# Kernel tuning notes

Hardware: AMD Instinct MI355X
Metric: run time of the kernel (lower is better)

The kernel has to match this reference:

```python
import jax, jax.numpy as jnp
import numpy as np

# DBMLLoss hyperparameters (from cfg.LOSSES.DBML_LOSS.*)
POS_A, POS_B = 1.0, 0.5
NEG_A, NEG_B = 0.6, 0.5
MARGIN, WEIGHT = 0.1, 0.5
EPS = 1e-5


def setup_inputs() -> dict:
    key = jax.random.key(0)
    k1, k2 = jax.random.split(key)
    feats = jax.random.normal(k1, (4096, 512), dtype=jnp.float32)
    feats = feats / jnp.linalg.norm(feats, axis=1, keepdims=True)  # metric-learning embeddings are L2-normalized
    labels = jax.random.randint(k2, (4096,), 0, 100)
    return {"feats": feats, "labels": labels}


def _dbml_loss(feats, labels):
    # feats: [B, D], labels: [B] int
    B = feats.shape[0]
    ninf = jnp.array(-jnp.inf, feats.dtype)
    pinf = jnp.array(jnp.inf, feats.dtype)

    sim = feats @ feats.T  # [B, B]
    same = labels[:, None] == labels[None, :]  # [B, B]
    # pos_pair_: same label and sim < 1 - eps (drops self-similarity of normalized feats)
    pos_mask = same & (sim < 1.0 - EPS)
    neg_mask = ~same

    # full-row stats (torch.mean(sum(...)) over a scalar == the sum)
    mean_all = sim.mean(axis=1)                               # [B]
    sigma_all = ((sim - mean_all[:, None]) ** 2).sum(axis=1)  # [B]

    max_neg = jnp.max(jnp.where(neg_mask, sim, ninf), axis=1)  # [B]
    min_pos = jnp.min(jnp.where(pos_mask, sim, pinf), axis=1)  # [B]

    # adaptive selection (adaptive_neg=True branch)
    pos_sel = pos_mask & (sim - MARGIN < max_neg[:, None])
    neg_sel = neg_mask & (sim + MARGIN > min_pos[:, None])

    n_pos = pos_sel.sum(axis=1)
    n_neg = neg_sel.sum(axis=1)
    valid = (pos_mask.sum(axis=1) > 0) & (neg_mask.sum(axis=1) > 0) & (n_pos > 0) & (n_neg > 0)

    sel = pos_sel | neg_sel
    cnt = jnp.maximum(n_pos + n_neg, 1).astype(sim.dtype)     # guard div-by-0 on invalid rows
    mean_sel = jnp.where(sel, sim, 0.0).sum(axis=1) / cnt
    sigma_sel = jnp.where(sel, (sim - mean_sel[:, None]) ** 2, 0.0).sum(axis=1) / cnt

    # fp = 1 + sum exp(-(pos - pos_a)/pos_b); fn = 1 + sum exp((neg - neg_a)/neg_b)
    fp = 1.0 + jnp.exp(jnp.where(pos_sel, -(sim - POS_A) / POS_B, ninf)).sum(axis=1)
    fn = 1.0 + jnp.exp(jnp.where(neg_sel, (sim - NEG_A) / NEG_B, ninf)).sum(axis=1)

    loss_i = (jnp.log(fp) + jnp.log(fn)
              + WEIGHT * (jnp.abs(mean_all - mean_sel) + jnp.abs(sigma_all - sigma_sel)))
    return jnp.where(valid, loss_i, 0.0).sum() / B


def reference(feats, labels):
    return _dbml_loss(feats, labels)
```

## Files before the change

### kernel.cpp

```cpp
#include <hip/hip_runtime.h>
#include <stdint.h>


#define Bn 4096
#define Dk 512
#define NCHUNK 8
#define CWIDTH 512
#define BM 128
#define TBN 128
#define BK 64
#define ONE_EPS 0.99999f

typedef short bf16x8 __attribute__((ext_vector_type(8)));
typedef float f32x4 __attribute__((ext_vector_type(4)));

__device__ __forceinline__ unsigned short f2bf(float x) {
  unsigned int u = __float_as_uint(x);
  u += 0x7fffu + ((u >> 16) & 1u);
  return (unsigned short)(u >> 16);
}

__global__ __launch_bounds__(256) void convert_kernel(const float* __restrict__ feats,
                                                      unsigned short* __restrict__ featT) {
  int g = blockIdx.x * 256 + threadIdx.x;
  int row = g & 4095;
  int kb = g >> 12;
  const float* src = feats + (size_t)row * Dk + kb * 8;
  f32x4 f0 = *(const f32x4*)(src);
  f32x4 f1 = *(const f32x4*)(src + 4);
  union { unsigned short u[8]; bf16x8 v; } o;
  o.u[0] = f2bf(f0[0]); o.u[1] = f2bf(f0[1]); o.u[2] = f2bf(f0[2]); o.u[3] = f2bf(f0[3]);
  o.u[4] = f2bf(f1[0]); o.u[5] = f2bf(f1[1]); o.u[6] = f2bf(f1[2]); o.u[7] = f2bf(f1[3]);
  *(bf16x8*)(featT + (size_t)g * 8) = o.v;
}

template <int PHASE>
__global__ __launch_bounds__(512, 2) void phase_kernel(const unsigned short* __restrict__ featT,
                                                       const int* __restrict__ labels,
                                                       const float* __restrict__ rs,
                                                       float* __restrict__ part) {
  __shared__ short As[1024 * 8];
  __shared__ short Bs[1024 * 8];
  __shared__ int rl[BM];
  __shared__ int cl[CWIDTH];

  const int tid = threadIdx.x;
  const int wid = tid >> 6;
  const int lane = tid & 63;
  const int WR = wid & 3;
  const int WC = wid >> 2;
  const int l15 = lane & 15;
  const int l4 = lane >> 4;
  const int row0 = blockIdx.x * BM;
  const int chunk0 = blockIdx.y * CWIDTH;

  for (int i = tid; i < BM; i += 512) rl[i] = labels[row0 + i];
  for (int i = tid; i < CWIDTH; i += 512) cl[i] = labels[chunk0 + i];
  __syncthreads();

  int rlab[2][4], rowl[2][4];
#pragma unroll
  for (int m = 0; m < 2; ++m)
#pragma unroll
    for (int r = 0; r < 4; ++r) {
      int lr = WR * 32 + m * 16 + l4 * 4 + r;
      rowl[m][r] = lr;
      rlab[m][r] = rl[lr];
    }

  float thrp[2][4], thrn[2][4];
  if constexpr (PHASE == 2) {
#pragma unroll
    for (int m = 0; m < 2; ++m)
#pragma unroll
      for (int r = 0; r < 4; ++r) {
        thrp[m][r] = rs[2 * Bn + row0 + rowl[m][r]];
        thrn[m][r] = rs[3 * Bn + row0 + rowl[m][r]];
      }
  }

  float s0[2][4], s1[2][4], s2[2][4], s3[2][4], s4[2][4], s5[2][4];
#pragma unroll
  for (int m = 0; m < 2; ++m)
#pragma unroll
    for (int r = 0; r < 4; ++r) {
      s0[m][r] = 0.f; s1[m][r] = 0.f;
      s2[m][r] = (PHASE == 1) ? -__builtin_inff() : 0.f;
      s3[m][r] = (PHASE == 1) ? __builtin_inff() : 0.f;
      s4[m][r] = 0.f; s5[m][r] = 0.f;
    }

  const int q0 = wid * 64 + lane;

  for (int ct = 0; ct < 4; ++ct) {
    const int col0 = chunk0 + ct * TBN;
    f32x4 acc[2][4];
#pragma unroll
    for (int m = 0; m < 2; ++m)
#pragma unroll
      for (int n = 0; n < 4; ++n) acc[m][n] = (f32x4){0.f, 0.f, 0.f, 0.f};

    for (int kt = 0; kt < Dk / BK; ++kt) {
      bf16x8 ra[2], rb[2];
#pragma unroll
      for (int i = 0; i < 2; ++i) {
        int q = q0 + i * 512;
        int r = q & 127;
        int kb = q >> 7;
        size_t koff = (size_t)(kt * 8 + kb) * Bn * 8;
        ra[i] = *(const bf16x8*)(featT + koff + (size_t)(row0 + r) * 8);
        rb[i] = *(const bf16x8*)(featT + koff + (size_t)(col0 + r) * 8);
      }
      __syncthreads();
#pragma unroll
      for (int i = 0; i < 2; ++i) {
        int q = q0 + i * 512;
        *(bf16x8*)&As[q * 8] = ra[i];
        *(bf16x8*)&Bs[q * 8] = rb[i];
      }
      __syncthreads();
#pragma unroll
      for (int ks = 0; ks < 2; ++ks) {
        const int kb = ks * 4 + l4;
        bf16x8 a[2], b[4];
#pragma unroll
        for (int m = 0; m < 2; ++m)
          a[m] = *(const bf16x8*)&As[(kb * 128 + WR * 32 + m * 16 + l15) * 8];
#pragma unroll
        for (int n = 0; n < 4; ++n)
          b[n] = *(const bf16x8*)&Bs[(kb * 128 + WC * 64 + n * 16 + l15) * 8];
#pragma unroll
        for (int m = 0; m < 2; ++m)
#pragma unroll
          for (int n = 0; n < 4; ++n)
            acc[m][n] = __builtin_amdgcn_mfma_f32_16x16x32_bf16(a[m], b[n], acc[m][n], 0, 0, 0);
      }
    }

    const bool diag = (col0 == row0);
    int clab[4], lcolt[4];
#pragma unroll
    for (int n = 0; n < 4; ++n) {
      lcolt[n] = WC * 64 + n * 16 + l15;
      clab[n] = cl[ct * TBN + lcolt[n]];
    }
#pragma unroll
    for (int m = 0; m < 2; ++m)
#pragma unroll
      for (int n = 0; n < 4; ++n)
#pragma unroll
        for (int r = 0; r < 4; ++r) {
          float s = acc[m][n][r];
          if (diag && (lcolt[n] == rowl[m][r])) s = 1.0f;
          bool same = (rlab[m][r] == clab[n]);
          if constexpr (PHASE == 1) {
            s0[m][r] += s;
            s1[m][r] += s * s;
            if (!same) s2[m][r] = fmaxf(s2[m][r], s);
            else if (s < ONE_EPS) { s3[m][r] = fminf(s3[m][r], s); s4[m][r] += 1.0f; }
          } else {
            bool psel = same && (s < ONE_EPS) && (s - 0.1f < thrp[m][r]);
            bool nsel = (!same) && (s + 0.1f > thrn[m][r]);
            if (psel) { s0[m][r] += 1.0f; s4[m][r] += __expf(2.0f - 2.0f * s); }
            if (nsel) { s1[m][r] += 1.0f; s5[m][r] += __expf(2.0f * s - 1.2f); }
            if (psel || nsel) { s2[m][r] += s; s3[m][r] += s * s; }
          }
        }
  }

#pragma unroll
  for (int d = 1; d < 16; d <<= 1) {
#pragma unroll
    for (int m = 0; m < 2; ++m)
#pragma unroll
      for (int r = 0; r < 4; ++r) {
        s0[m][r] += __shfl_xor(s0[m][r], d);
        s1[m][r] += __shfl_xor(s1[m][r], d);
        if constexpr (PHASE == 1) {
          s2[m][r] = fmaxf(s2[m][r], __shfl_xor(s2[m][r], d));
          s3[m][r] = fminf(s3[m][r], __shfl_xor(s3[m][r], d));
          s4[m][r] += __shfl_xor(s4[m][r], d);
        } else {
          s2[m][r] += __shfl_xor(s2[m][r], d);
          s3[m][r] += __shfl_xor(s3[m][r], d);
          s4[m][r] += __shfl_xor(s4[m][r], d);
          s5[m][r] += __shfl_xor(s5[m][r], d);
        }
      }
  }

  if (l15 == 0) {
    const int slot = blockIdx.y * 2 + WC;
#pragma unroll
    for (int m = 0; m < 2; ++m)
#pragma unroll
      for (int r = 0; r < 4; ++r) {
        int rowg = row0 + rowl[m][r];
        part[(size_t)(0 * Bn + rowg) * 16 + slot] = s0[m][r];
        part[(size_t)(1 * Bn + rowg) * 16 + slot] = s1[m][r];
        part[(size_t)(2 * Bn + rowg) * 16 + slot] = s2[m][r];
        part[(size_t)(3 * Bn + rowg) * 16 + slot] = s3[m][r];
        part[(size_t)(4 * Bn + rowg) * 16 + slot] = s4[m][r];
        if constexpr (PHASE == 2)
          part[(size_t)(5 * Bn + rowg) * 16 + slot] = s5[m][r];
      }
  }
}

__global__ __launch_bounds__(256) void reduce1_kernel(const float* __restrict__ part,
                                                      float* __restrict__ rs) {
  int row = blockIdx.x * 256 + threadIdx.x;
  float sum = 0.f, ssq = 0.f, pc = 0.f;
  float mxn = -__builtin_inff(), mnp = __builtin_inff();
#pragma unroll
  for (int sl = 0; sl < 16; ++sl) {
    sum += part[(size_t)(0 * Bn + row) * 16 + sl];
    ssq += part[(size_t)(1 * Bn + row) * 16 + sl];
    mxn = fmaxf(mxn, part[(size_t)(2 * Bn + row) * 16 + sl]);
    mnp = fminf(mnp, part[(size_t)(3 * Bn + row) * 16 + sl]);
    pc += part[(size_t)(4 * Bn + row) * 16 + sl];
  }
  rs[0 * Bn + row] = sum;
  rs[1 * Bn + row] = ssq;
  rs[2 * Bn + row] = mxn;
  rs[3 * Bn + row] = mnp;
  rs[4 * Bn + row] = pc;
}

__global__ __launch_bounds__(256) void finalize_kernel(const float* __restrict__ p2,
                                                       const float* __restrict__ rs,
                                                       float* __restrict__ out) {
  int tid = threadIdx.x;
  int row = blockIdx.x * 256 + tid;
  float np = 0.f, nn = 0.f, ssel = 0.f, qsel = 0.f, fp = 0.f, fn = 0.f;
#pragma unroll
  for (int sl = 0; sl < 16; ++sl) {
    np += p2[(size_t)(0 * Bn + row) * 16 + sl];
    nn += p2[(size_t)(1 * Bn + row) * 16 + sl];
    ssel += p2[(size_t)(2 * Bn + row) * 16 + sl];
    qsel += p2[(size_t)(3 * Bn + row) * 16 + sl];
    fp += p2[(size_t)(4 * Bn + row) * 16 + sl];
    fn += p2[(size_t)(5 * Bn + row) * 16 + sl];
  }
  float sumall = rs[0 * Bn + row];
  float ssqall = rs[1 * Bn + row];
  float pc = rs[4 * Bn + row];

  float mean_all = sumall * (1.0f / Bn);
  float sigma_all = ssqall - (float)Bn * mean_all * mean_all;
  float cnt = fmaxf(np + nn, 1.0f);
  float mean_sel = ssel / cnt;
  float sigma_sel = qsel / cnt - mean_sel * mean_sel;
  float loss = __logf(1.0f + fp) + __logf(1.0f + fn) +
               0.5f * (fabsf(mean_all - mean_sel) + fabsf(sigma_all - sigma_sel));
  bool valid = (pc > 0.5f) && (pc < (float)(Bn - 1) - 0.5f) && (np > 0.5f) && (nn > 0.5f);
  float v = valid ? loss : 0.f;
#pragma unroll
  for (int d = 1; d < 64; d <<= 1) v += __shfl_xor(v, d);
  __shared__ float ls[4];
  if ((tid & 63) == 0) ls[tid >> 6] = v;
  __syncthreads();
  if (tid == 0) atomicAdd(out, (ls[0] + ls[1] + ls[2] + ls[3]) * (1.0f / (float)Bn));
}

extern "C" void kernel_launch(void* const* d_in, const int* in_sizes, int n_in,
                              void* d_out, int out_size, void* d_ws, size_t ws_size,
                              hipStream_t stream) {
  const float* feats = (const float*)d_in[0];
  const int* labels = (const int*)d_in[1];
  float* out = (float*)d_out;
  char* ws = (char*)d_ws;

  unsigned short* featT = (unsigned short*)(ws);
  float* p1 = (float*)(ws + 4194304);
  float* rs = (float*)(ws + 4194304 + 1310720);
  float* p2 = (float*)(ws + 4194304 + 1310720 + 81920);

  hipMemsetAsync(d_out, 0, sizeof(float), stream);
  convert_kernel<<<1024, 256, 0, stream>>>(feats, featT);
  dim3 g(Bn / BM, NCHUNK);
  phase_kernel<1><<<g, 512, 0, stream>>>(featT, labels, nullptr, p1);
  reduce1_kernel<<<Bn / 256, 256, 0, stream>>>(p1, rs);
  phase_kernel<2><<<g, 512, 0, stream>>>(featT, labels, rs, p2);
  finalize_kernel<<<Bn / 256, 256, 0, stream>>>(p2, rs, out);
}
```

Measured before the change: 150.2 us.

## Double-buffer LDS tiles with direct global-to-LDS loads and halve column chunk width

New measurement: 205.2 us. 36.6% more time.

```diff
diff --git a/kernel.cpp b/kernel.cpp
--- a/kernel.cpp
+++ b/kernel.cpp
@@ -4,11 +4,12 @@
 
 #define Bn 4096
 #define Dk 512
-#define NCHUNK 8
-#define CWIDTH 512
+#define NCHUNK 16
+#define CWIDTH 256
 #define BM 128
 #define TBN 128
 #define BK 64
+#define NSTEP 16
 #define ONE_EPS 0.99999f
 
 typedef short bf16x8 __attribute__((ext_vector_type(8)));
@@ -34,13 +35,19 @@
   *(bf16x8*)(featT + (size_t)g * 8) = o.v;
 }
 
+__device__ __forceinline__ void gload16(const unsigned short* g, short* l) {
+  __builtin_amdgcn_global_load_lds((const __attribute__((address_space(1))) unsigned int*)g,
+                                   (__attribute__((address_space(3))) unsigned int*)l,
+                                   16, 0, 0);
+}
+
 template <int PHASE>
-__global__ __launch_bounds__(512, 2) void phase_kernel(const unsigned short* __restrict__ featT,
+__global__ __launch_bounds__(512, 4) void phase_kernel(const unsigned short* __restrict__ featT,
                                                        const int* __restrict__ labels,
                                                        const float* __restrict__ rs,
                                                        float* __restrict__ part) {
-  __shared__ short As[1024 * 8];
-  __shared__ short Bs[1024 * 8];
+  __shared__ short As[2][8192];
+  __shared__ short Bs[2][8192];
   __shared__ int rl[BM];
   __shared__ int cl[CWIDTH];
 
@@ -54,30 +61,22 @@
   const int row0 = blockIdx.x * BM;
   const int chunk0 = blockIdx.y * CWIDTH;
 
-  for (int i = tid; i < BM; i += 512) rl[i] = labels[row0 + i];
-  for (int i = tid; i < CWIDTH; i += 512) cl[i] = labels[chunk0 + i];
-  __syncthreads();
+  if (tid < BM) rl[tid] = labels[row0 + tid];
+  if (tid < CWIDTH) cl[tid] = labels[chunk0 + tid];
 
   int rlab[2][4], rowl[2][4];
+  float thrp[2][4], thrn[2][4];
 #pragma unroll
   for (int m = 0; m < 2; ++m)
 #pragma unroll
     for (int r = 0; r < 4; ++r) {
       int lr = WR * 32 + m * 16 + l4 * 4 + r;
       rowl[m][r] = lr;
-      rlab[m][r] = rl[lr];
-    }
-
-  float thrp[2][4], thrn[2][4];
-  if constexpr (PHASE == 2) {
-#pragma unroll
-    for (int m = 0; m < 2; ++m)
-#pragma unroll
-      for (int r = 0; r < 4; ++r) {
-        thrp[m][r] = rs[2 * Bn + row0 + rowl[m][r]];
-        thrn[m][r] = rs[3 * Bn + row0 + rowl[m][r]];
-      }
-  }
+      if constexpr (PHASE == 2) {
+        thrp[m][r] = rs[2 * Bn + row0 + lr];
+        thrn[m][r] = rs[3 * Bn + row0 + lr];
+      }
+    }
 
   float s0[2][4], s1[2][4], s2[2][4], s3[2][4], s4[2][4], s5[2][4];
 #pragma unroll
@@ -90,9 +89,30 @@
       s4[m][r] = 0.f; s5[m][r] = 0.f;
     }
 
-  const int q0 = wid * 64 + lane;
-
-  for (int ct = 0; ct < 4; ++ct) {
+  auto stage = [&](int s) {
+    const int ct = s >> 3, kt = s & 7, bb = s & 1;
+    const int cbase = chunk0 + ct * TBN;
+#pragma unroll
+    for (int i = 0; i < 2; ++i) {
+      const int q = tid + i * 512;
+      const int r = q & 127;
+      const int kb = q >> 7;
+      const int ko = (kt * 8 + kb) * (Bn * 8);
+      gload16(featT + ko + (row0 + r) * 8, &As[bb][q * 8]);
+      gload16(featT + ko + (cbase + r) * 8, &Bs[bb][q * 8]);
+    }
+  };
+
+  stage(0);
+
+#pragma unroll
+  for (int m = 0; m < 2; ++m)
+#pragma unroll
+    for (int r = 0; r < 4; ++r) {
+      rlab[m][r] = 0;
+    }
+
+  for (int ct = 0; ct < CWIDTH / TBN; ++ct) {
     const int col0 = chunk0 + ct * TBN;
     f32x4 acc[2][4];
 #pragma unroll
@@ -101,39 +121,31 @@
       for (int n = 0; n < 4; ++n) acc[m][n] = (f32x4){0.f, 0.f, 0.f, 0.f};
 
     for (int kt = 0; kt < Dk / BK; ++kt) {
-      bf16x8 ra[2], rb[2];
-#pragma unroll
-      for (int i = 0; i < 2; ++i) {
-        int q = q0 + i * 512;
-        int r = q & 127;
-        int kb = q >> 7;
-        size_t koff = (size_t)(kt * 8 + kb) * Bn * 8;
-        ra[i] = *(const bf16x8*)(featT + koff + (size_t)(row0 + r) * 8);
-        rb[i] = *(const bf16x8*)(featT + koff + (size_t)(col0 + r) * 8);
-      }
+      const int s = ct * 8 + kt;
       __syncthreads();
-#pragma unroll
-      for (int i = 0; i < 2; ++i) {
-        int q = q0 + i * 512;
-        *(bf16x8*)&As[q * 8] = ra[i];
-        *(bf16x8*)&Bs[q * 8] = rb[i];
-      }
-      __syncthreads();
+      if (s + 1 < NSTEP) stage(s + 1);
+      if (s == 0) {
+#pragma unroll
+        for (int m = 0; m < 2; ++m)
+#pragma unroll
+          for (int r = 0; r < 4; ++r) rlab[m][r] = rl[rowl[m][r]];
+      }
+      const int bb = s & 1;
 #pragma unroll
       for (int ks = 0; ks < 2; ++ks) {
         const int kb = ks * 4 + l4;
-        bf16x8 a[2], b[4];
+        bf16x8 af[2], bf[4];
 #pragma unroll
         for (int m = 0; m < 2; ++m)
-          a[m] = *(const bf16x8*)&As[(kb * 128 + WR * 32 + m * 16 + l15) * 8];
+          af[m] = *(const bf16x8*)&As[bb][(kb * 128 + WR * 32 + m * 16 + l15) * 8];
 #pragma unroll
         for (int n = 0; n < 4; ++n)
-          b[n] = *(const bf16x8*)&Bs[(kb * 128 + WC * 64 + n * 16 + l15) * 8];
+          bf[n] = *(const bf16x8*)&Bs[bb][(kb * 128 + WC * 64 + n * 16 + l15) * 8];
 #pragma unroll
         for (int m = 0; m < 2; ++m)
 #pragma unroll
           for (int n = 0; n < 4; ++n)
-            acc[m][n] = __builtin_amdgcn_mfma_f32_16x16x32_bf16(a[m], b[n], acc[m][n], 0, 0, 0);
+            acc[m][n] = __builtin_amdgcn_mfma_f32_16x16x32_bf16(af[m], bf[n], acc[m][n], 0, 0, 0);
       }
     }
 
@@ -189,20 +201,49 @@
       }
   }
 
-  if (l15 == 0) {
-    const int slot = blockIdx.y * 2 + WC;
+  __syncthreads();
+  float* mbuf = (float*)&As[0][0];
+  if (WC == 1 && l15 == 0) {
 #pragma unroll
     for (int m = 0; m < 2; ++m)
 #pragma unroll
       for (int r = 0; r < 4; ++r) {
-        int rowg = row0 + rowl[m][r];
-        part[(size_t)(0 * Bn + rowg) * 16 + slot] = s0[m][r];
-        part[(size_t)(1 * Bn + rowg) * 16 + slot] = s1[m][r];
-        part[(size_t)(2 * Bn + rowg) * 16 + slot] = s2[m][r];
-        part[(size_t)(3 * Bn + rowg) * 16 + slot] = s3[m][r];
-        part[(size_t)(4 * Bn + rowg) * 16 + slot] = s4[m][r];
+        int lr = rowl[m][r];
+        mbuf[lr * 6 + 0] = s0[m][r];
+        mbuf[lr * 6 + 1] = s1[m][r];
+        mbuf[lr * 6 + 2] = s2[m][r];
+        mbuf[lr * 6 + 3] = s3[m][r];
+        mbuf[lr * 6 + 4] = s4[m][r];
+        mbuf[lr * 6 + 5] = s5[m][r];
+      }
+  }
+  __syncthreads();
+  if (WC == 0 && l15 == 0) {
+    const int slot = blockIdx.y;
+#pragma unroll
+    for (int m = 0; m < 2; ++m)
+#pragma unroll
+      for (int r = 0; r < 4; ++r) {
+        int lr = rowl[m][r];
+        int rowg = row0 + lr;
+        float t0 = s0[m][r] + mbuf[lr * 6 + 0];
+        float t1 = s1[m][r] + mbuf[lr * 6 + 1];
+        float t2, t3;
+        if constexpr (PHASE == 1) {
+          t2 = fmaxf(s2[m][r], mbuf[lr * 6 + 2]);
+          t3 = fminf(s3[m][r], mbuf[lr * 6 + 3]);
+        } else {
+          t2 = s2[m][r] + mbuf[lr * 6 + 2];
+          t3 = s3[m][r] + mbuf[lr * 6 + 3];
+        }
+        float t4 = s4[m][r] + mbuf[lr * 6 + 4];
+        part[(size_t)(0 * Bn + rowg) * 16 + slot] = t0;
+        part[(size_t)(1 * Bn + rowg) * 16 + slot] = t1;
+        part[(size_t)(2 * Bn + rowg) * 16 + slot] = t2;
+        part[(size_t)(3 * Bn + rowg) * 16 + slot] = t3;
+        part[(size_t)(4 * Bn + rowg) * 16 + slot] = t4;
         if constexpr (PHASE == 2)
-          part[(size_t)(5 * Bn + rowg) * 16 + slot] = s5[m][r];
+          part[(size_t)(5 * Bn + rowg) * 16 + slot] = s5[m][r] + mbuf[lr * 6 + 5];
       }
   }
 }
```
